# Kernel tuning notes

Measured on AMD Instinct MI355X. Metric: run time of the kernel, lower is better.

## Reference

```python
import jax, jax.numpy as jnp
import numpy as np

G, S, P = 128, 32, 16          # graphs, subgraphs per graph, nodes per subgraph
D, C, NH, OUT = 768, 256, 4, 7 # input dim, hidden dim, GAT heads, classes


def setup_inputs() -> dict:
    key = jax.random.key(0)
    ks = jax.random.split(key, 17)
    n = lambda k, shape, s=0.05: jax.random.normal(k, shape, dtype=jnp.float32) * s
    return {
        "x": jax.random.normal(ks[0], (G, S, P, D), dtype=jnp.float32),
        # GATConv(768 -> 256, heads=4, concat=False): lin weight, att vectors, bias
        "gat_W": n(ks[1], (D, NH * C)),
        "att_src": n(ks[2], (NH, C)),
        "att_dst": n(ks[3], (NH, C)),
        "gat_b": n(ks[4], (C,)),
        # GRU(256 -> 256), torch layout [3*H, in]
        "gru_Wih": n(ks[5], (3 * C, C)),
        "gru_Whh": n(ks[6], (3 * C, C)),
        "gru_bih": n(ks[7], (3 * C,)),
        "gru_bhh": n(ks[8], (3 * C,)),
        # scale_up_projection Linear(256 -> 768)
        "up_W": n(ks[9], (D, C)),
        "up_b": n(ks[10], (D,)),
        # speaker_projection Linear(1536 -> 768) + ReLU
        "sp_W": n(ks[11], (D, 2 * D)),
        "sp_b": n(ks[12], (D,)),
        # GlobalAttention gate Linear(256 -> 1)
        "att_W": n(ks[13], (1, C)),
        "att_b": n(ks[14], (1,)),
        # classifier Linear(256 -> 7)
        "cls_W": n(ks[15], (OUT, C)),
        "cls_b": n(ks[16], (OUT,)),
    }


def _gat(x, W, a_src, a_dst, b):
    # PyG GATConv on a star graph (speaker = local node 0 -> all others) with
    # default add_self_loops=True, negative_slope=0.2, concat=False (mean over heads).
    # x: [G, P, D]
    h = jnp.einsum('gpd,dhc->gphc', x, W.reshape(D, NH, C))     # per-head transform
    es = jnp.sum(h * a_src, -1)                                 # [G, P, NH]
    ed = jnp.sum(h * a_dst, -1)
    lrelu = lambda v: jnp.where(v > 0, v, 0.2 * v)
    e_spk = lrelu(es[:, :1] + ed)   # edge speaker -> t
    e_slf = lrelu(es + ed)          # self loop t -> t
    w = jax.nn.softmax(jnp.stack([e_spk, e_slf], -1), axis=-1)  # [G, P, NH, 2]
    # for t == 0 both terms are h[:,0] and weights sum to 1, matching the
    # speaker node receiving only its self loop.
    out = w[..., 0:1] * h[:, :1] + w[..., 1:2] * h              # [G, P, NH, C]
    return out.mean(axis=2) + b


def _gru_cell(xin, h, Wih, Whh, bih, bhh):
    gi = xin @ Wih.T + bih
    gh = h @ Whh.T + bhh
    ir, iz, inn = jnp.split(gi, 3, -1)
    hr, hz, hn = jnp.split(gh, 3, -1)
    r = jax.nn.sigmoid(ir + hr)
    z = jax.nn.sigmoid(iz + hz)
    return (1 - z) * jnp.tanh(inn + r * hn) + z * h


def _forward(x, gat_W, att_src, att_dst, gat_b, gru_Wih, gru_Whh, gru_bih, gru_bhh,
             up_W, up_b, sp_W, sp_b, att_W, att_b, cls_W, cls_b):
    g, s, p, d = x.shape
    m0 = _gat(x[:, 0], gat_W, att_src, att_dst, gat_b)  # [G, P, C]
    h0 = jnp.zeros((g, p, C), x.dtype)

    def step(carry, _):
        h_run, m_prev = carry
        # running GRU hidden over memory prefix, then one zero-input step
        # (equivalent to rerunning the GRU over [m_0..m_{j-1}, 0])
        h_run = _gru_cell(m_prev, h_run, gru_Wih, gru_Whh, gru_bih, gru_bhh)
        h_nxt = _gru_cell(jnp.zeros_like(h_run), h_run, gru_Wih, gru_Whh, gru_bih, gru_bhh)
        pooled = h_nxt @ up_W.T + up_b                  # [G, P, D]
        # faithful to source: non_speaker_indices covers ALL nodes (torch.equal
        # shape-mismatch bug), and speaker_info is read AFTER the overwrite,
        # so the speaker concat is [pooled, pooled] and raw x[:, j>=1] is unused.
        spk = jnp.concatenate([pooled[:, 0], pooled[:, 0]], -1)  # [G, 2D]
        spk = jax.nn.relu(spk @ sp_W.T + sp_b)
        x_new = pooled.at[:, 0].set(spk)
        m = _gat(x_new, gat_W, att_src, att_dst, gat_b)
        return (h_run, m), m

    (_, _), ms = jax.lax.scan(step, (h0, m0), None, length=s - 1)
    mem = jnp.concatenate([m0[None], ms], axis=0)        # [S, G, P, C]
    # GlobalAttention pool over the P nodes of each subgraph memory state
    gate = jax.nn.softmax(jnp.squeeze(mem @ att_W.T + att_b, -1), axis=-1)  # [S, G, P]
    pooled = jnp.einsum('sgp,sgpc->sgc', gate, mem)
    logits = pooled @ cls_W.T + cls_b                    # [S, G, OUT]
    # torch stacks graph-major: [G*S, 1, OUT]
    return jnp.transpose(logits, (1, 0, 2)).reshape(g * s, 1, OUT)


def reference(x, gat_W, att_src, att_dst, gat_b, gru_Wih, gru_Whh, gru_bih, gru_bhh,
              up_W, up_b, sp_W, sp_b, att_W, att_b, cls_W, cls_b):
    return _forward(x, gat_W, att_src, att_dst, gat_b, gru_Wih, gru_Whh, gru_bih,
                    gru_bhh, up_W, up_b, sp_W, sp_b, att_W, att_b, cls_W, cls_b)
```

## Files before the change

### kernel.cpp

```cpp
#include <hip/hip_runtime.h>
#include <math.h>

#define NG 128
#define NS 32
#define NP 16
#define ND 768
#define NC 256
#define NHD 4
#define NOUT 7
#define NR 2048

typedef unsigned short ushortT;
typedef short bf16x8 __attribute__((ext_vector_type(8)));
typedef float f32x4 __attribute__((ext_vector_type(4)));

__device__ __forceinline__ ushortT f2b(float f) {
    union { float f; unsigned u; } v; v.f = f;
    unsigned r = (v.u + 0x7FFF + ((v.u >> 16) & 1)) >> 16;
    return (ushortT)r;
}
__device__ __forceinline__ float sigf(float v) { return 1.f / (1.f + expf(-v)); }

#define MFMA16(a, b, c) __builtin_amdgcn_mfma_f32_16x16x32_bf16((a), (b), (c), 0, 0, 0)

__global__ __launch_bounds__(256) void bgemm_kernel(
    const ushortT* __restrict__ A, const ushortT* __restrict__ Asub,
    const ushortT* __restrict__ Bt, const float* __restrict__ bias,
    float* __restrict__ outF, ushortT* __restrict__ outH,
    int N, int K, int act)
{
    __shared__ short As[64 * 40];
    __shared__ short Bs[64 * 40];
    const int tid = threadIdx.x;
    const int lane = tid & 63, wid = tid >> 6;
    const int quad = lane >> 4, l15 = lane & 15;
    const int row0 = blockIdx.y * 64, col0 = blockIdx.x * 64;
    const int mh = (wid & 1) * 32, nh = (wid >> 1) * 32;
    const int sr = tid >> 2, skq = (tid & 3) * 8;
    const int grow_s = row0 + sr;
    const ushortT* aptr = (Asub && ((grow_s & 15) == 0))
        ? Asub + (size_t)(grow_s >> 4) * K : A + (size_t)grow_s * K;
    const ushortT* bptr = Bt + (size_t)(col0 + sr) * K;

    f32x4 acc[2][2];
    for (int i = 0; i < 2; ++i)
        for (int j = 0; j < 2; ++j) acc[i][j] = (f32x4){0.f, 0.f, 0.f, 0.f};

    for (int kk = 0; kk < K; kk += 32) {
        __syncthreads();
        *(uint4*)&As[sr * 40 + skq] = *(const uint4*)(aptr + kk + skq);
        *(uint4*)&Bs[sr * 40 + skq] = *(const uint4*)(bptr + kk + skq);
        __syncthreads();
        bf16x8 af0 = *(const bf16x8*)&As[(mh + l15) * 40 + quad * 8];
        bf16x8 af1 = *(const bf16x8*)&As[(mh + 16 + l15) * 40 + quad * 8];
        bf16x8 bf0 = *(const bf16x8*)&Bs[(nh + l15) * 40 + quad * 8];
        bf16x8 bf1 = *(const bf16x8*)&Bs[(nh + 16 + l15) * 40 + quad * 8];
        acc[0][0] = MFMA16(af0, bf0, acc[0][0]);
        acc[0][1] = MFMA16(af0, bf1, acc[0][1]);
        acc[1][0] = MFMA16(af1, bf0, acc[1][0]);
        acc[1][1] = MFMA16(af1, bf1, acc[1][1]);
    }
#pragma unroll
    for (int mt = 0; mt < 2; ++mt)
#pragma unroll
        for (int nt = 0; nt < 2; ++nt) {
            const int gc = col0 + nh + nt * 16 + l15;
            const float bv = bias ? bias[gc] : 0.f;
#pragma unroll
            for (int r = 0; r < 4; ++r) {
                const int gr = row0 + mh + mt * 16 + quad * 4 + r;
                float v = acc[mt][nt][r] + bv;
                if (act) v = fmaxf(v, 0.f);
                if (outF) outF[(size_t)gr * N + gc] = v;
                if (outH) outH[(size_t)gr * N + gc] = f2b(v);
            }
        }
}

__global__ __launch_bounds__(256) void gru1_mfma_kernel(
    const ushortT* __restrict__ mB, const ushortT* __restrict__ hB,
    const ushortT* __restrict__ WihB, const ushortT* __restrict__ WhhB,
    const float* __restrict__ bih, const float* __restrict__ bhh,
    float* __restrict__ hF, ushortT* __restrict__ hBout)
{
    __shared__ short As[2 * 32 * 264];
    __shared__ short Bs[384 * 40];
    const int tid = threadIdx.x;
    const int lane = tid & 63, wid = tid >> 6;
    const int quad = lane >> 4, l15 = lane & 15;
    const int row0 = blockIdx.y * 32;
    const int n0 = blockIdx.x * 64;
    const int mt = wid & 1, nhh = (wid >> 1) * 32;

    for (int c = tid; c < 2048; c += 256) {
        const int mat = c >> 10, r2 = c & 1023, row = r2 >> 5, kc = (r2 & 31) * 8;
        const ushortT* src = (mat ? hB : mB) + (size_t)(row0 + row) * NC + kc;
        *(uint4*)&As[mat * 8448 + row * 264 + kc] = *(const uint4*)src;
    }
    f32x4 acc[2][3][2];
    for (int w = 0; w < 2; ++w)
        for (int g = 0; g < 3; ++g)
            for (int n = 0; n < 2; ++n) acc[w][g][n] = (f32x4){0.f, 0.f, 0.f, 0.f};

    for (int kk = 0; kk < 256; kk += 32) {
        __syncthreads();
        for (int c = tid; c < 1536; c += 256) {
            const int j = c >> 2, kq = (c & 3) * 8;
            const int w = j / 192, j2 = j - w * 192, gt = j2 >> 6, nloc = j2 & 63;
            const ushortT* src = (w ? WhhB : WihB) +
                (size_t)(gt * 256 + n0 + nloc) * NC + kk + kq;
            *(uint4*)&Bs[j * 40 + kq] = *(const uint4*)src;
        }
        __syncthreads();
        bf16x8 af0 = *(const bf16x8*)&As[(mt * 16 + l15) * 264 + kk + quad * 8];
        bf16x8 af1 = *(const bf16x8*)&As[8448 + (mt * 16 + l15) * 264 + kk + quad * 8];
#pragma unroll
        for (int gt = 0; gt < 3; ++gt)
#pragma unroll
            for (int nt = 0; nt < 2; ++nt) {
                const int jb = gt * 64 + nhh + nt * 16 + l15;
                bf16x8 b0 = *(const bf16x8*)&Bs[jb * 40 + quad * 8];
                bf16x8 b1 = *(const bf16x8*)&Bs[(192 + jb) * 40 + quad * 8];
                acc[0][gt][nt] = MFMA16(af0, b0, acc[0][gt][nt]);
                acc[1][gt][nt] = MFMA16(af1, b1, acc[1][gt][nt]);
            }
    }
#pragma unroll
    for (int nt = 0; nt < 2; ++nt) {
        const int c = n0 + nhh + nt * 16 + l15;
        const float br = bih[c], bz = bih[256 + c], bn = bih[512 + c];
        const float cr = bhh[c], cz = bhh[256 + c], cn = bhh[512 + c];
#pragma unroll
        for (int r = 0; r < 4; ++r) {
            const int grow = row0 + mt * 16 + quad * 4 + r;
            const size_t idx = (size_t)grow * NC + c;
            const float hold = hF[idx];
            const float rg = sigf(acc[0][0][nt][r] + br + acc[1][0][nt][r] + cr);
            const float zg = sigf(acc[0][1][nt][r] + bz + acc[1][1][nt][r] + cz);
            const float ng = tanhf(acc[0][2][nt][r] + bn + rg * (acc[1][2][nt][r] + cn));
            const float hn = (1.f - zg) * ng + zg * hold;
            hF[idx] = hn;
            hBout[idx] = f2b(hn);
        }
    }
}

__global__ __launch_bounds__(256) void gru2_mfma_kernel(
    const ushortT* __restrict__ hB, const ushortT* __restrict__ WhhB,
    const float* __restrict__ bih, const float* __restrict__ bhh,
    const float* __restrict__ hF, ushortT* __restrict__ hnB,
    ushortT* __restrict__ h0c)
{
    __shared__ short As[32 * 264];
    __shared__ short Bs[192 * 40];
    const int tid = threadIdx.x;
    const int lane = tid & 63, wid = tid >> 6;
    const int quad = lane >> 4, l15 = lane & 15;
    const int row0 = blockIdx.y * 32;
    const int n0 = blockIdx.x * 64;
    const int mt = wid & 1, nhh = (wid >> 1) * 32;

    for (int c = tid; c < 1024; c += 256) {
        const int row = c >> 5, kc = (c & 31) * 8;
        *(uint4*)&As[row * 264 + kc] =
            *(const uint4*)(hB + (size_t)(row0 + row) * NC + kc);
    }
    f32x4 acc[3][2];
    for (int g = 0; g < 3; ++g)
        for (int n = 0; n < 2; ++n) acc[g][n] = (f32x4){0.f, 0.f, 0.f, 0.f};

    for (int kk = 0; kk < 256; kk += 32) {
        __syncthreads();
        for (int c = tid; c < 768; c += 256) {
            const int j = c >> 2, kq = (c & 3) * 8;
            const int gt = j >> 6, nloc = j & 63;
            *(uint4*)&Bs[j * 40 + kq] =
                *(const uint4*)(WhhB + (size_t)(gt * 256 + n0 + nloc) * NC + kk + kq);
        }
        __syncthreads();
        bf16x8 af = *(const bf16x8*)&As[(mt * 16 + l15) * 264 + kk + quad * 8];
#pragma unroll
        for (int gt = 0; gt < 3; ++gt)
#pragma unroll
            for (int nt = 0; nt < 2; ++nt) {
                const int jb = gt * 64 + nhh + nt * 16 + l15;
                bf16x8 b = *(const bf16x8*)&Bs[jb * 40 + quad * 8];
                acc[gt][nt] = MFMA16(af, b, acc[gt][nt]);
            }
    }
#pragma unroll
    for (int nt = 0; nt < 2; ++nt) {
        const int c = n0 + nhh + nt * 16 + l15;
        const float br = bih[c], bz = bih[256 + c], bn = bih[512 + c];
        const float cr = bhh[c], cz = bhh[256 + c], cn = bhh[512 + c];
#pragma unroll
        for (int r = 0; r < 4; ++r) {
            const int grow = row0 + mt * 16 + quad * 4 + r;
            const size_t idx = (size_t)grow * NC + c;
            const float rg = sigf(br + acc[0][nt][r] + cr);
            const float zg = sigf(bz + acc[1][nt][r] + cz);
            const float ng = tanhf(bn + rg * (acc[2][nt][r] + cn));
            const float hv = (1.f - zg) * ng + zg * hF[idx];
            const ushortT hb = f2b(hv);
            hnB[idx] = hb;
            if ((grow & 15) == 0) h0c[(size_t)(grow >> 4) * NC + c] = hb;
        }
    }
}

__global__ __launch_bounds__(256) void fin_kernel(
    const float* __restrict__ hbuf, const float* __restrict__ att_src,
    const float* __restrict__ att_dst, const float* __restrict__ gat_b,
    const float* __restrict__ attW, const float* __restrict__ attb,
    const float* __restrict__ clsW, const float* __restrict__ clsb,
    ushortT* __restrict__ mB, float* __restrict__ outp, int s)
{
    const int g = blockIdx.x, tid = threadIdx.x;
    const int lane = tid & 63, wid = tid >> 6;
    __shared__ float es_s[16][4], ed_s[16][4];
    __shared__ float m_s[16][260];
    __shared__ float gate_s[16];
    __shared__ float pooled_s[256];
    const float* hb = hbuf + (size_t)g * NP * (NHD * NC);

    for (int pi = 0; pi < 4; ++pi) {
        const int p = wid * 4 + pi;
        const float* row = hb + p * (NHD * NC);
        float ss[4] = {0.f, 0.f, 0.f, 0.f}, sd[4] = {0.f, 0.f, 0.f, 0.f};
#pragma unroll
        for (int i = 0; i < 16; ++i) {
            const int col = lane + 64 * i;
            const float v = row[col];
            ss[i >> 2] += v * att_src[col];
            sd[i >> 2] += v * att_dst[col];
        }
        for (int off = 32; off; off >>= 1)
#pragma unroll
            for (int h = 0; h < 4; ++h) {
                ss[h] += __shfl_down(ss[h], off);
                sd[h] += __shfl_down(sd[h], off);
            }
        if (lane == 0)
#pragma unroll
            for (int h = 0; h < 4; ++h) { es_s[p][h] = ss[h]; ed_s[p][h] = sd[h]; }
    }
    __syncthreads();
    {
        const int p = tid >> 4, cb = (tid & 15) * 16;
        float accv[16];
#pragma unroll
        for (int cj = 0; cj < 16; ++cj) accv[cj] = 0.f;
#pragma unroll
        for (int h = 0; h < 4; ++h) {
            float e1 = es_s[0][h] + ed_s[p][h]; e1 = e1 > 0.f ? e1 : 0.2f * e1;
            float e2 = es_s[p][h] + ed_s[p][h]; e2 = e2 > 0.f ? e2 : 0.2f * e2;
            const float mx = fmaxf(e1, e2);
            float w0 = expf(e1 - mx), w1 = expf(e2 - mx);
            const float inv = 1.f / (w0 + w1);
            w0 *= inv; w1 *= inv;
            const float* r0 = hb + h * NC + cb;
            const float* rp = hb + p * (NHD * NC) + h * NC + cb;
#pragma unroll
            for (int cj = 0; cj < 16; ++cj) accv[cj] += w0 * r0[cj] + w1 * rp[cj];
        }
#pragma unroll
        for (int cj = 0; cj < 16; ++cj) {
            const float v = accv[cj] * 0.25f + gat_b[cb + cj];
            m_s[p][cb + cj] = v;
            mB[(size_t)(g * NP + p) * NC + cb + cj] = f2b(v);
        }
    }
    __syncthreads();
    for (int pi = 0; pi < 4; ++pi) {
        const int p = wid * 4 + pi;
        float sg = 0.f;
#pragma unroll
        for (int i = 0; i < 4; ++i) { const int c = lane + 64 * i; sg += m_s[p][c] * attW[c]; }
        for (int off = 32; off; off >>= 1) sg += __shfl_down(sg, off);
        if (lane == 0) gate_s[p] = sg + attb[0];
    }
    __syncthreads();
    float mx = -1e30f;
#pragma unroll
    for (int p = 0; p < 16; ++p) mx = fmaxf(mx, gate_s[p]);
    float ge[16], ssum = 0.f;
#pragma unroll
    for (int p = 0; p < 16; ++p) { ge[p] = expf(gate_s[p] - mx); ssum += ge[p]; }
    const float inv = 1.f / ssum;
    {
        float pc = 0.f;
#pragma unroll
        for (int p = 0; p < 16; ++p) pc += ge[p] * m_s[p][tid];
        pooled_s[tid] = pc * inv;
    }
    __syncthreads();
    const int o = tid >> 5, l32 = tid & 31;
    if (o < NOUT) {
        float a = 0.f;
#pragma unroll
        for (int i = 0; i < 8; ++i) {
            const int c = l32 + 32 * i;
            a += pooled_s[c] * clsW[o * NC + c];
        }
        for (int off = 16; off; off >>= 1) a += __shfl_down(a, off);
        if (l32 == 0) outp[((size_t)g * NS + s) * NOUT + o] = a + clsb[o];
    }
}

__global__ __launch_bounds__(256) void cast_kernel(const float* __restrict__ a,
                                                   ushortT* __restrict__ b, int n) {
    const int i = blockIdx.x * 256 + threadIdx.x;
    if (i < n) b[i] = f2b(a[i]);
}
__global__ __launch_bounds__(256) void gatT_kernel(const float* __restrict__ gW,
                                                   ushortT* __restrict__ gB) {
    const int idx = blockIdx.x * 256 + threadIdx.x;
    const int c = idx / ND, d = idx - c * ND;
    gB[idx] = f2b(gW[(size_t)d * (NHD * NC) + c]);
}
__global__ __launch_bounds__(256) void spwc_kernel(const float* __restrict__ spW,
                                                   float* __restrict__ o) {
    const int idx = blockIdx.x * 256 + threadIdx.x;
    const int r = idx / ND, d = idx - r * ND;
    o[idx] = spW[(size_t)r * (2 * ND) + d] + spW[(size_t)r * (2 * ND) + ND + d];
}
__global__ __launch_bounds__(256) void wus_kernel(const float* __restrict__ spWc,
                                                  const float* __restrict__ upW,
                                                  ushortT* __restrict__ WusB) {
    const int c = threadIdx.x;
    const int o0 = blockIdx.x * 16;
    float acc[16];
#pragma unroll
    for (int i = 0; i < 16; ++i) acc[i] = 0.f;
    for (int d = 0; d < ND; ++d) {
        const float u = upW[(size_t)d * NC + c];
#pragma unroll
        for (int i = 0; i < 16; ++i) acc[i] += spWc[(size_t)(o0 + i) * ND + d] * u;
    }
#pragma unroll
    for (int i = 0; i < 16; ++i) WusB[(size_t)(o0 + i) * NC + c] = f2b(acc[i]);
}
__global__ __launch_bounds__(256) void bus_kernel(const float* __restrict__ spWc,
                                                  const float* __restrict__ up_b,
                                                  const float* __restrict__ sp_b,
                                                  float* __restrict__ bus) {
    const int o = blockIdx.x * 256 + threadIdx.x;
    if (o >= ND) return;
    float a = sp_b[o];
    const float* sr = spWc + (size_t)o * ND;
    for (int d = 0; d < ND; ++d) a += sr[d] * up_b[d];
    bus[o] = a;
}
__global__ __launch_bounds__(256) void x0_kernel(const float* __restrict__ x,
                                                 ushortT* __restrict__ xb) {
    const int idx = blockIdx.x * 256 + threadIdx.x;
    const int row = idx / ND, d = idx - row * ND;
    const int g = row >> 4, p = row & 15;
    xb[idx] = f2b(x[((size_t)g * (NS * NP) + p) * ND + d]);
}
__global__ __launch_bounds__(256) void zh_kernel(float* hF, ushortT* hB) {
    const int idx = blockIdx.x * 256 + threadIdx.x;
    hF[idx] = 0.f;
    hB[idx] = 0;
}

extern "C" void kernel_launch(void* const* d_in, const int* in_sizes, int n_in,
                              void* d_out, int out_size, void* d_ws, size_t ws_size,
                              hipStream_t stream) {
    (void)in_sizes; (void)n_in; (void)out_size; (void)ws_size;
    const float* x       = (const float*)d_in[0];
    const float* gat_W   = (const float*)d_in[1];
    const float* att_src = (const float*)d_in[2];
    const float* att_dst = (const float*)d_in[3];
    const float* gat_b   = (const float*)d_in[4];
    const float* gru_Wih = (const float*)d_in[5];
    const float* gru_Whh = (const float*)d_in[6];
    const float* gru_bih = (const float*)d_in[7];
    const float* gru_bhh = (const float*)d_in[8];
    const float* up_W    = (const float*)d_in[9];
    const float* up_b    = (const float*)d_in[10];
    const float* sp_W    = (const float*)d_in[11];
    const float* sp_b    = (const float*)d_in[12];
    const float* att_W   = (const float*)d_in[13];
    const float* att_b   = (const float*)d_in[14];
    const float* cls_W   = (const float*)d_in[15];
    const float* cls_b   = (const float*)d_in[16];
    float* outp = (float*)d_out;

    char* w = (char*)d_ws;
    ushortT* xb    = (ushortT*)w; w += (size_t)NR * ND * 2;
    ushortT* WihB  = (ushortT*)w; w += (size_t)(3 * NC) * NC * 2;
    ushortT* WhhB  = (ushortT*)w; w += (size_t)(3 * NC) * NC * 2;
    ushortT* upWB  = (ushortT*)w; w += (size_t)ND * NC * 2;
    ushortT* gatB  = (ushortT*)w; w += (size_t)(NHD * NC) * ND * 2;
    ushortT* WusB  = (ushortT*)w; w += (size_t)ND * NC * 2;
    float*   spWc  = (float*)w;   w += (size_t)ND * ND * 4;
    float*   bus   = (float*)w;   w += (size_t)ND * 4;
    float*   hF    = (float*)w;   w += (size_t)NR * NC * 4;
    ushortT* hB    = (ushortT*)w; w += (size_t)NR * NC * 2;
    ushortT* hnB   = (ushortT*)w; w += (size_t)NR * NC * 2;
    ushortT* h0c   = (ushortT*)w; w += (size_t)NG * NC * 2;
    ushortT* poolB = (ushortT*)w; w += (size_t)NR * ND * 2;
    ushortT* spkB  = (ushortT*)w; w += (size_t)NG * ND * 2;
    float*   hbuf  = (float*)w;   w += (size_t)NR * (NHD * NC) * 4;
    ushortT* mB    = (ushortT*)w; w += (size_t)NR * NC * 2;

    cast_kernel<<<768, 256, 0, stream>>>(gru_Wih, WihB, 3 * NC * NC);
    cast_kernel<<<768, 256, 0, stream>>>(gru_Whh, WhhB, 3 * NC * NC);
    cast_kernel<<<768, 256, 0, stream>>>(up_W, upWB, ND * NC);
    gatT_kernel<<<(NHD * NC * ND) / 256, 256, 0, stream>>>(gat_W, gatB);
    spwc_kernel<<<(ND * ND) / 256, 256, 0, stream>>>(sp_W, spWc);
    wus_kernel<<<ND / 16, 256, 0, stream>>>(spWc, up_W, WusB);
    bus_kernel<<<3, 256, 0, stream>>>(spWc, up_b, sp_b, bus);
    x0_kernel<<<(NR * ND) / 256, 256, 0, stream>>>(x, xb);
    zh_kernel<<<(NR * NC) / 256, 256, 0, stream>>>(hF, hB);

    bgemm_kernel<<<dim3((NHD * NC) / 64, NR / 64), 256, 0, stream>>>(
        xb, nullptr, gatB, nullptr, hbuf, nullptr, NHD * NC, ND, 0);
    fin_kernel<<<NG, 256, 0, stream>>>(hbuf, att_src, att_dst, gat_b,
                                       att_W, att_b, cls_W, cls_b, mB, outp, 0);

    for (int j = 1; j < NS; ++j) {
        gru1_mfma_kernel<<<dim3(NC / 64, NR / 32), 256, 0, stream>>>(
            mB, hB, WihB, WhhB, gru_bih, gru_bhh, hF, hB);
        gru2_mfma_kernel<<<dim3(NC / 64, NR / 32), 256, 0, stream>>>(
            hB, WhhB, gru_bih, gru_bhh, hF, hnB, h0c);
        bgemm_kernel<<<dim3(ND / 64, NR / 64), 256, 0, stream>>>(
            hnB, nullptr, upWB, up_b, nullptr, poolB, ND, NC, 0);
        bgemm_kernel<<<dim3(ND / 64, NG / 64), 256, 0, stream>>>(
            h0c, nullptr, WusB, bus, nullptr, spkB, ND, NC, 1);
        bgemm_kernel<<<dim3((NHD * NC) / 64, NR / 64), 256, 0, stream>>>(
            poolB, spkB, gatB, nullptr, hbuf, nullptr, NHD * NC, ND, 0);
        fin_kernel<<<NG, 256, 0, stream>>>(hbuf, att_src, att_dst, gat_b,
                                           att_W, att_b, cls_W, cls_b, mB, outp, j);
    }
}
```

Baseline: 2.642 ms.

## Fold up-projection into GAT weight to skip per-step 768-dim pooled GEMM

After: 2.630 ms. About the same (-0.5%).

```diff
diff --git a/kernel.cpp b/kernel.cpp
--- a/kernel.cpp
+++ b/kernel.cpp
@@ -24,10 +24,9 @@
 #define MFMA16(a, b, c) __builtin_amdgcn_mfma_f32_16x16x32_bf16((a), (b), (c), 0, 0, 0)
 
 __global__ __launch_bounds__(256) void bgemm_kernel(
-    const ushortT* __restrict__ A, const ushortT* __restrict__ Asub,
-    const ushortT* __restrict__ Bt, const float* __restrict__ bias,
-    float* __restrict__ outF, ushortT* __restrict__ outH,
-    int N, int K, int act)
+    const ushortT* __restrict__ A, const ushortT* __restrict__ Bt,
+    const float* __restrict__ bias, float* __restrict__ outF,
+    ushortT* __restrict__ outH, int N, int K, int act, int rowStride)
 {
     __shared__ short As[64 * 40];
     __shared__ short Bs[64 * 40];
@@ -37,9 +36,7 @@
     const int row0 = blockIdx.y * 64, col0 = blockIdx.x * 64;
     const int mh = (wid & 1) * 32, nh = (wid >> 1) * 32;
     const int sr = tid >> 2, skq = (tid & 3) * 8;
-    const int grow_s = row0 + sr;
-    const ushortT* aptr = (Asub && ((grow_s & 15) == 0))
-        ? Asub + (size_t)(grow_s >> 4) * K : A + (size_t)grow_s * K;
+    const ushortT* aptr = A + (size_t)(row0 + sr) * K;
     const ushortT* bptr = Bt + (size_t)(col0 + sr) * K;
 
     f32x4 acc[2][2];
@@ -68,7 +65,7 @@
             const float bv = bias ? bias[gc] : 0.f;
 #pragma unroll
             for (int r = 0; r < 4; ++r) {
-                const int gr = row0 + mh + mt * 16 + quad * 4 + r;
+                const int gr = (row0 + mh + mt * 16 + quad * 4 + r) * rowStride;
                 float v = acc[mt][nt][r] + bv;
                 if (act) v = fmaxf(v, 0.f);
                 if (outF) outF[(size_t)gr * N + gc] = v;
@@ -317,6 +314,21 @@
     const int idx = blockIdx.x * 256 + threadIdx.x;
     const int c = idx / ND, d = idx - c * ND;
     gB[idx] = f2b(gW[(size_t)d * (NHD * NC) + c]);
+}
+__global__ __launch_bounds__(256) void upwT_kernel(const float* __restrict__ upW,
+                                                   ushortT* __restrict__ o) {
+    const int idx = blockIdx.x * 256 + threadIdx.x;
+    const int k = idx / ND, d = idx - k * ND;
+    o[idx] = f2b(upW[(size_t)d * NC + k]);
+}
+__global__ __launch_bounds__(256) void bcomb_kernel(const float* __restrict__ gW,
+                                                    const float* __restrict__ up_b,
+                                                    float* __restrict__ bc) {
+    const int c = blockIdx.x * 256 + threadIdx.x;
+    if (c >= NHD * NC) return;
+    float a = 0.f;
+    for (int d = 0; d < ND; ++d) a += up_b[d] * gW[(size_t)d * (NHD * NC) + c];
+    bc[c] = a;
 }
 __global__ __launch_bounds__(256) void spwc_kernel(const float* __restrict__ spW,
                                                    float* __restrict__ o) {
@@ -391,32 +403,36 @@
     ushortT* xb    = (ushortT*)w; w += (size_t)NR * ND * 2;
     ushortT* WihB  = (ushortT*)w; w += (size_t)(3 * NC) * NC * 2;
     ushortT* WhhB  = (ushortT*)w; w += (size_t)(3 * NC) * NC * 2;
-    ushortT* upWB  = (ushortT*)w; w += (size_t)ND * NC * 2;
     ushortT* gatB  = (ushortT*)w; w += (size_t)(NHD * NC) * ND * 2;
     ushortT* WusB  = (ushortT*)w; w += (size_t)ND * NC * 2;
+    ushortT* upWT  = (ushortT*)w; w += (size_t)NC * ND * 2;
+    ushortT* WcombB= (ushortT*)w; w += (size_t)(NHD * NC) * NC * 2;
+    float*   bcomb = (float*)w;   w += (size_t)(NHD * NC) * 4;
     float*   spWc  = (float*)w;   w += (size_t)ND * ND * 4;
     float*   bus   = (float*)w;   w += (size_t)ND * 4;
     float*   hF    = (float*)w;   w += (size_t)NR * NC * 4;
     ushortT* hB    = (ushortT*)w; w += (size_t)NR * NC * 2;
     ushortT* hnB   = (ushortT*)w; w += (size_t)NR * NC * 2;
     ushortT* h0c   = (ushortT*)w; w += (size_t)NG * NC * 2;
-    ushortT* poolB = (ushortT*)w; w += (size_t)NR * ND * 2;
     ushortT* spkB  = (ushortT*)w; w += (size_t)NG * ND * 2;
     float*   hbuf  = (float*)w;   w += (size_t)NR * (NHD * NC) * 4;
     ushortT* mB    = (ushortT*)w; w += (size_t)NR * NC * 2;
 
     cast_kernel<<<768, 256, 0, stream>>>(gru_Wih, WihB, 3 * NC * NC);
     cast_kernel<<<768, 256, 0, stream>>>(gru_Whh, WhhB, 3 * NC * NC);
-    cast_kernel<<<768, 256, 0, stream>>>(up_W, upWB, ND * NC);
     gatT_kernel<<<(NHD * NC * ND) / 256, 256, 0, stream>>>(gat_W, gatB);
+    upwT_kernel<<<(NC * ND) / 256, 256, 0, stream>>>(up_W, upWT);
+    bcomb_kernel<<<(NHD * NC) / 256, 256, 0, stream>>>(gat_W, up_b, bcomb);
     spwc_kernel<<<(ND * ND) / 256, 256, 0, stream>>>(sp_W, spWc);
     wus_kernel<<<ND / 16, 256, 0, stream>>>(spWc, up_W, WusB);
     bus_kernel<<<3, 256, 0, stream>>>(spWc, up_b, sp_b, bus);
     x0_kernel<<<(NR * ND) / 256, 256, 0, stream>>>(x, xb);
     zh_kernel<<<(NR * NC) / 256, 256, 0, stream>>>(hF, hB);
+    bgemm_kernel<<<dim3(NC / 64, (NHD * NC) / 64), 256, 0, stream>>>(
+        gatB, upWT, nullptr, nullptr, WcombB, NC, ND, 0, 1);
 
     bgemm_kernel<<<dim3((NHD * NC) / 64, NR / 64), 256, 0, stream>>>(
-        xb, nullptr, gatB, nullptr, hbuf, nullptr, NHD * NC, ND, 0);
+        xb, gatB, nullptr, hbuf, nullptr, NHD * NC, ND, 0, 1);
     fin_kernel<<<NG, 256, 0, stream>>>(hbuf, att_src, att_dst, gat_b,
                                        att_W, att_b, cls_W, cls_b, mB, outp, 0);
 
@@ -425,12 +441,12 @@
             mB, hB, WihB, WhhB, gru_bih, gru_bhh, hF, hB);
         gru2_mfma_kernel<<<dim3(NC / 64, NR / 32), 256, 0, stream>>>(
             hB, WhhB, gru_bih, gru_bhh, hF, hnB, h0c);
-        bgemm_kernel<<<dim3(ND / 64, NR / 64), 256, 0, stream>>>(
-            hnB, nullptr, upWB, up_b, nullptr, poolB, ND, NC, 0);
         bgemm_kernel<<<dim3(ND / 64, NG / 64), 256, 0, stream>>>(
-            h0c, nullptr, WusB, bus, nullptr, spkB, ND, NC, 1);
+            h0c, WusB, bus, nullptr, spkB, ND, NC, 1, 1);
         bgemm_kernel<<<dim3((NHD * NC) / 64, NR / 64), 256, 0, stream>>>(
-            poolB, spkB, gatB, nullptr, hbuf, nullptr, NHD * NC, ND, 0);
+            hnB, WcombB, bcomb, hbuf, nullptr, NHD * NC, NC, 0, 1);
+        bgemm_kernel<<<dim3((NHD * NC) / 64, NG / 64), 256, 0, stream>>>(
+            spkB, gatB, nullptr, hbuf, nullptr, NHD * NC, ND, 0, 16);
         fin_kernel<<<NG, 256, 0, stream>>>(hbuf, att_src, att_dst, gat_b,
                                            att_W, att_b, cls_W, cls_b, mB, outp, j);
     }
```
